# Kernel tuning notes

Hardware: AMD Instinct MI355X
Metric: run time of the kernel (lower is better)

Reference implementation:

```python
import jax, jax.numpy as jnp
import numpy as np

B, M, K = 32768, 8192, 16
EPS = 1e-5  # torch BatchNorm1d default


def _bn_relu(x, g, b):
    # training-mode batch norm (biased variance), matching torch BatchNorm1d forward
    m = x.mean(0)
    v = x.var(0)
    return jax.nn.relu(g * (x - m) * jax.lax.rsqrt(v + EPS) + b)


def _forward(pos, mc, mv, w1, b1, w2, b2, w3, b3, w4, b4, w5, b5, w6, b6,
             g1, be1, g2, be2, g3, be3, g4, be4, g5, be5, k):
    # squared pairwise distances [B, M]; same ordering as L2 norm used by torch.sort
    d2 = (pos * pos).sum(1, keepdims=True) + (mc * mc).sum(1)[None, :] - 2.0 * (pos @ mc.T)
    _, idx = jax.lax.top_k(-d2, k)                     # k nearest indices [B, k]
    nb = jnp.concatenate([mc[idx], mv[idx]], axis=-1)  # [B, k, 4] = (coord, value) per neighbor
    knn_feat = jnp.concatenate([pos, nb.reshape(pos.shape[0], k * 4)], axis=1)  # [B, 2+4k]
    x = _bn_relu(knn_feat @ w1 + b1, g1, be1)
    x = _bn_relu(x @ w2 + b2, g2, be2)
    x = _bn_relu(x @ w3 + b3, g3, be3)
    x = _bn_relu(x @ w4 + b4, g4, be4)
    x = _bn_relu(x @ w5 + b5, g5, be5)  # dropout = identity (eval mode)
    x = x @ w6 + b6
    return x, knn_feat


def setup_inputs() -> dict:
    key = jax.random.key(0)
    ks = jax.random.split(key, 32)
    d_in = 2 + K * 4
    dims = [(d_in, 128), (128, 256), (256, 512), (512, 128), (128, 64), (64, 2)]
    inp = {
        "pos": jax.random.normal(ks[0], (B, 2), jnp.float32),
        "measure_coords": jax.random.normal(ks[1], (M, 2), jnp.float32),
        "measure_vals": jax.random.normal(ks[2], (M, 2), jnp.float32),
    }
    for i, (fi, fo) in enumerate(dims, 1):
        inp[f"w{i}"] = jax.random.normal(ks[2 + 2 * i], (fi, fo), jnp.float32) / np.float32(np.sqrt(fi))
        inp[f"b{i}"] = jnp.zeros((fo,), jnp.float32)
    for i, n in enumerate([128, 256, 512, 128, 64], 1):
        inp[f"g{i}"] = jnp.ones((n,), jnp.float32)
        inp[f"be{i}"] = jnp.zeros((n,), jnp.float32)
    inp["k"] = K
    return inp


def reference(pos, measure_coords, measure_vals, w1, b1, w2, b2, w3, b3, w4, b4,
              w5, b5, w6, b6, g1, be1, g2, be2, g3, be3, g4, be4, g5, be5, k):
    return _forward(pos, measure_coords, measure_vals, w1, b1, w2, b2, w3, b3, w4,
                    b4, w5, b5, w6, b6, g1, be1, g2, be2, g3, be3, g4, be4, g5, be5, k)
```

## Files before the change

### kernel.cpp

```cpp
#include <hip/hip_runtime.h>

typedef unsigned short u16;
typedef unsigned int   u32;
typedef __attribute__((ext_vector_type(8))) short bf16x8;
typedef __attribute__((ext_vector_type(4))) float f32x4;

#define B_ROWS 32768
#define EPS_BN 1e-5f

__device__ __forceinline__ u16 f2bf(float f) {
  u32 u = __float_as_uint(f);
  u32 r = (u + 0x7FFFu + ((u >> 16) & 1u)) >> 16;
  return (u16)r;
}
__device__ __forceinline__ u32 pk2bf(float a, float b) {
  return (u32)f2bf(a) | ((u32)f2bf(b) << 16);
}
__device__ __forceinline__ float bf2f(u16 h) {
  return __uint_as_float(((u32)h) << 16);
}

__device__ __forceinline__ float dcalc(float px, float py, float sp, float mx, float my) {
#pragma clang fp contract(off)
  float sm   = mx * mx + my * my;
  float pm   = px * mx;
  float dot  = __builtin_fmaf(py, my, pm);
  float spsm = sp + sm;
  return __builtin_fmaf(dot, -2.0f, spsm);
}
__device__ __forceinline__ float dcalc2(float px, float py, float sp, float mx, float my,
                                        float sm) {
#pragma clang fp contract(off)
  float pm   = px * mx;
  float dot  = __builtin_fmaf(py, my, pm);
  float spsm = sp + sm;
  return __builtin_fmaf(dot, -2.0f, spsm);
}
__device__ __forceinline__ float smcalc(float mx, float my) {
#pragma clang fp contract(off)
  return mx * mx + my * my;
}
__device__ __forceinline__ float spcalc(float px, float py) {
#pragma clang fp contract(off)
  return px * px + py * py;
}
#define MED3 __builtin_amdgcn_fmed3f

__global__ __launch_bounds__(256, 8)
void knn_kernel(const float2* __restrict__ pos, const float2* __restrict__ mc,
                const float2* __restrict__ mv, float* __restrict__ knn_out,
                u16* __restrict__ X0)
{
  __shared__ float tv[16 * 65];
  __shared__ float tstS[16];
  __shared__ float qxS[16], qyS[16], qsS[16];
  __shared__ unsigned long long qmaskS[16];
  __shared__ int   qcnt[16];
  __shared__ int   ntaskS;

  const int t = threadIdx.x;
  const int g = t >> 6;
  const int s = t & 63;
  const int q0 = blockIdx.x * 16;

  float px[4], py[4], sp[4];
#pragma unroll
  for (int j = 0; j < 4; ++j) {
    float2 p = pos[q0 + g * 4 + j];
    px[j] = p.x; py[j] = p.y; sp[j] = spcalc(p.x, p.y);
  }
#pragma unroll
  for (int j = 0; j < 4; ++j) {
    if (s == j) { qxS[g * 4 + j] = px[j]; qyS[g * 4 + j] = py[j]; qsS[g * 4 + j] = sp[j]; }
  }

  const float4* mc4 = (const float4*)mc;

  float z0a[4], z0b[4];
#pragma unroll
  for (int j = 0; j < 4; ++j) { z0a[j] = __builtin_inff(); z0b[j] = __builtin_inff(); }

  float4 cur = mc4[s];
  for (int i = 0; i < 64; ++i) {
    float4 nxt = mc4[((i + 1) & 63) * 64 + s];
    float smA = smcalc(cur.x, cur.y);
    float smB = smcalc(cur.z, cur.w);
#pragma unroll
    for (int j = 0; j < 4; ++j) {
      float dA = dcalc2(px[j], py[j], sp[j], cur.x, cur.y, smA);
      z0a[j] = fminf(z0a[j], dA);
      float dB = dcalc2(px[j], py[j], sp[j], cur.z, cur.w, smB);
      z0b[j] = fminf(z0b[j], dB);
    }
    cur = nxt;
  }
  float z0[4];
#pragma unroll
  for (int j = 0; j < 4; ++j) {
    z0[j] = fminf(z0a[j], z0b[j]);
    tv[(g * 4 + j) * 65 + s] = z0[j];
  }
  __syncthreads();

  if (t < 16) {
    float ch[16];
#pragma unroll
    for (int j = 0; j < 16; ++j) ch[j] = __builtin_inff();
    for (int k = 0; k < 64; ++k) {
      float v = tv[t * 65 + k];
#pragma unroll
      for (int j = 15; j >= 1; --j) ch[j] = MED3(ch[j-1], v, ch[j]);
      ch[0] = fminf(ch[0], v);
    }
    tstS[t] = ch[15];
    qcnt[t] = 0;
    if (t == 0) ntaskS = 0;
  }
  __syncthreads();

  {
    float Tq[4];
#pragma unroll
    for (int j = 0; j < 4; ++j) Tq[j] = tstS[g * 4 + j];
    unsigned long long m;
#pragma unroll
    for (int j = 0; j < 4; ++j) {
      m = __ballot(z0[j] <= Tq[j]);
      if (s == j) qmaskS[g * 4 + j] = m;
    }
  }
  __syncthreads();

  u16* qcand = (u16*)tv;
  u16* taskS = ((u16*)tv) + 1024;
  if (t < 16) {
    unsigned long long m = qmaskS[t];
    int c = __popcll(m);
    int off = atomicAdd(&ntaskS, c);
    u16 qb = (u16)(t << 6);
    while (m) {
      int b = (int)__builtin_ctzll(m);
      m &= m - 1;
      taskS[off++] = qb | (u16)b;
    }
  }
  __syncthreads();

  const int ntask = ntaskS;
  for (int i0 = t; i0 < ntask; i0 += 256) {
    const int task = taskS[i0];
    const int qrow = task >> 6;
    const int sl   = task & 63;
    const float qx = qxS[qrow], qy = qyS[qrow];
    const float qs = qsS[qrow], qT = tstS[qrow];
#pragma unroll 4
    for (int i = 0; i < 64; ++i) {
      float4 c2 = mc4[i * 64 + sl];
      const int pidx = 2 * (i * 64 + sl);
      float smA = smcalc(c2.x, c2.y);
      float smB = smcalc(c2.z, c2.w);
      float dA = dcalc2(qx, qy, qs, c2.x, c2.y, smA);
      float dB = dcalc2(qx, qy, qs, c2.z, c2.w, smB);
      if (dA <= qT) {
        int o = atomicAdd(&qcnt[qrow], 1);
        if (o < 64) qcand[qrow * 64 + o] = (u16)pidx;
      }
      if (dB <= qT) {
        int o = atomicAdd(&qcnt[qrow], 1);
        if (o < 64) qcand[qrow * 64 + o] = (u16)(pidx + 1);
      }
    }
  }
  __syncthreads();

  if (t < 16) {
    const int q = q0 + t;
    float2 p = pos[q];
    const float sq = spcalc(p.x, p.y);
    int cnt = qcnt[t]; if (cnt > 64) cnt = 64;
    float fd[16]; int fi[16];
#pragma unroll
    for (int j = 0; j < 16; ++j) { fd[j] = __builtin_inff(); fi[j] = 0x7fffffff; }
    for (int j = 0; j < cnt; ++j) {
      int ci = qcand[t * 64 + j];
      float2 m = mc[ci];
      float d = dcalc(p.x, p.y, sq, m.x, m.y);
      bool cc = (d < fd[15]) || (d == fd[15] && ci < fi[15]);
      if (cc) {
#pragma unroll
        for (int k = 15; k >= 1; --k) {
          bool cm = (d < fd[k-1]) || (d == fd[k-1] && ci < fi[k-1]);
          if (cc) {
            if (cm) { fd[k] = fd[k-1]; fi[k] = fi[k-1]; }
            else    { fd[k] = d;       fi[k] = ci;      }
          }
          cc = cm;
        }
        if (cc) { fd[0] = d; fi[0] = ci; }
      }
    }
    float* orow = knn_out + (size_t)q * 66;
    u16*   xrow = X0 + (size_t)q * 96;
    float2 pp; pp.x = p.x; pp.y = p.y;
    *(float2*)(&orow[0]) = pp;
    *(u32*)(&xrow[0]) = pk2bf(p.x, p.y);
#pragma unroll
    for (int j = 0; j < 16; ++j) {
      int ci = fi[j];
      float2 m = mc[ci], v = mv[ci];
      *(float2*)(&orow[2 + 4*j]) = m;
      *(float2*)(&orow[4 + 4*j]) = v;
      *(u32*)(&xrow[2 + 4*j]) = pk2bf(m.x, m.y);
      *(u32*)(&xrow[4 + 4*j]) = pk2bf(v.x, v.y);
    }
#pragma unroll
    for (int c = 33; c < 48; ++c) ((u32*)xrow)[c] = 0;
  }
}

__global__ __launch_bounds__(256)
void prep_wt_all(const float* __restrict__ w1, const float* __restrict__ w2,
                 const float* __restrict__ w3, const float* __restrict__ w4,
                 const float* __restrict__ w5,
                 u16* __restrict__ wt1, u16* __restrict__ wt2, u16* __restrict__ wt3,
                 u16* __restrict__ wt4, u16* __restrict__ wt5)
{
  const int l = blockIdx.y;
  const float* w; u16* wt; int K, N, Kp;
  if (l == 0)      { w = w1; wt = wt1; K = 66;  N = 128; Kp = 96;  }
  else if (l == 1) { w = w2; wt = wt2; K = 128; N = 256; Kp = 128; }
  else if (l == 2) { w = w3; wt = wt3; K = 256; N = 512; Kp = 256; }
  else if (l == 3) { w = w4; wt = wt4; K = 512; N = 128; Kp = 512; }
  else             { w = w5; wt = wt5; K = 128; N = 64;  Kp = 128; }
  int i = blockIdx.x * 256 + threadIdx.x;
  if (i >= N * Kp) return;
  int n = i / Kp, kp = i - n * Kp;
  float v = (kp < K) ? w[(size_t)kp * N + n] : 0.0f;
  wt[i] = f2bf(v);
}

template<int KW, int BN, bool FUSE>
__global__ __launch_bounds__(256, 4)
void gemm_bn_kernel(const u16* __restrict__ X,
                    const u16* __restrict__ WT,
                    const float* __restrict__ bias,
                    const float* __restrict__ psum, const float* __restrict__ psq,
                    const float* __restrict__ gw,   const float* __restrict__ bw,
                    u16* __restrict__ Z, int N,
                    float* __restrict__ csum, float* __restrict__ csq)
{
  constexpr int BM = 128;
  constexpr int AST = 40;
  constexpr int NSTEP = KW / 32;
  __shared__ u16 Ash[2][BM * AST];
  __shared__ u16 Bsh[2][BN * AST];
  __shared__ float redS[4][BN];
  __shared__ float redQ[4][BN];
  __shared__ float scA[FUSE ? KW : 1];
  __shared__ float ttA[FUSE ? KW : 1];

  const int t = threadIdx.x;
  const int wave = t >> 6;
  const int lane = t & 63;
  const int lr = lane & 15;
  const int qd = lane >> 4;
  const int m0 = blockIdx.x * BM;
  const int n0 = blockIdx.y * BN;

  if (FUSE) {
    const float invB = 1.0f / 32768.0f;
    for (int c = t; c < KW; c += 256) {
      float mean = psum[c] * invB;
      float var  = __fmaf_rn(-mean, mean, psq[c] * invB);
      float sc   = gw[c] * rsqrtf(var + EPS_BN);
      scA[c] = sc;
      ttA[c] = __fmaf_rn(-mean, sc, bw[c]);
    }
    __syncthreads();
  }

  f32x4 acc[2][BN / 16];
#pragma unroll
  for (int a = 0; a < 2; ++a)
#pragma unroll
    for (int b = 0; b < BN / 16; ++b) {
      acc[a][b][0] = 0.f; acc[a][b][1] = 0.f; acc[a][b][2] = 0.f; acc[a][b][3] = 0.f;
    }

  const int sr = t >> 2;
  const int sk = (t & 3) * 8;

  const u16* Arow0 = &X[(size_t)(m0 + sr) * KW + sk];
  const u16* Arow1 = &X[(size_t)(m0 + sr + 64) * KW + sk];
  const u16* Brow  = &WT[(size_t)(n0 + sr) * KW + sk];

  auto fuseq = [&](uint4 gv, int kk) -> uint4 {
    u32 w[4] = {gv.x, gv.y, gv.z, gv.w};
    u32 o[4];
#pragma unroll
    for (int e = 0; e < 4; ++e) {
      float lo = bf2f((u16)(w[e] & 0xffffu));
      float hi = bf2f((u16)(w[e] >> 16));
      float yl = fmaxf(__fmaf_rn(lo, scA[kk + 2 * e],     ttA[kk + 2 * e]),     0.0f);
      float yh = fmaxf(__fmaf_rn(hi, scA[kk + 2 * e + 1], ttA[kk + 2 * e + 1]), 0.0f);
      o[e] = (u32)f2bf(yl) | ((u32)f2bf(yh) << 16);
    }
    uint4 r; r.x = o[0]; r.y = o[1]; r.z = o[2]; r.w = o[3];
    return r;
  };

  {
    uint4 a0 = *(const uint4*)(Arow0);
    uint4 a1 = *(const uint4*)(Arow1);
    uint4 b0 = *(const uint4*)(Brow);
    if (FUSE) { a0 = fuseq(a0, sk); a1 = fuseq(a1, sk); }
    *(uint4*)(&Ash[0][sr * AST + sk]) = a0;
    *(uint4*)(&Ash[0][(sr + 64) * AST + sk]) = a1;
    *(uint4*)(&Bsh[0][sr * AST + sk]) = b0;
  }
  uint4 a0n = {}, a1n = {}, b0n = {};
  if (NSTEP > 1) {
    a0n = *(const uint4*)(Arow0 + 32);
    a1n = *(const uint4*)(Arow1 + 32);
    b0n = *(const uint4*)(Brow + 32);
  }
  __syncthreads();

  for (int ts = 0; ts < NSTEP; ++ts) {
    const int cur = ts & 1;

    uint4 La0 = a0n, La1 = a1n, Lb0 = b0n;
    if (ts + 2 < NSTEP) {
      const int ko = (ts + 2) * 32;
      La0 = *(const uint4*)(Arow0 + ko);
      La1 = *(const uint4*)(Arow1 + ko);
      Lb0 = *(const uint4*)(Brow + ko);
    }

    bf16x8 af0 = *(const bf16x8*)(&Ash[cur][(wave * 32 + lr) * AST + qd * 8]);
    bf16x8 af1 = *(const bf16x8*)(&Ash[cur][(wave * 32 + 16 + lr) * AST + qd * 8]);
#pragma unroll
    for (int ct = 0; ct < BN / 16; ++ct) {
      bf16x8 bfr = *(const bf16x8*)(&Bsh[cur][(ct * 16 + lr) * AST + qd * 8]);
      acc[0][ct] = __builtin_amdgcn_mfma_f32_16x16x32_bf16(af0, bfr, acc[0][ct], 0, 0, 0);
      acc[1][ct] = __builtin_amdgcn_mfma_f32_16x16x32_bf16(af1, bfr, acc[1][ct], 0, 0, 0);
    }

    if (ts + 1 < NSTEP) {
      uint4 wa0 = a0n, wa1 = a1n, wb0 = b0n;
      if (FUSE) {
        const int kk = (ts + 1) * 32 + sk;
        wa0 = fuseq(wa0, kk);
        wa1 = fuseq(wa1, kk);
      }
      *(uint4*)(&Ash[cur ^ 1][sr * AST + sk]) = wa0;
      *(uint4*)(&Ash[cur ^ 1][(sr + 64) * AST + sk]) = wa1;
      *(uint4*)(&Bsh[cur ^ 1][sr * AST + sk]) = wb0;
      __syncthreads();
      a0n = La0; a1n = La1; b0n = Lb0;
    }
  }

#pragma unroll
  for (int ct = 0; ct < BN / 16; ++ct) {
    int cg = n0 + ct * 16 + lr;
    float bv = bias[cg];
    float s = 0.f, sqv = 0.f;
#pragma unroll
    for (int rt = 0; rt < 2; ++rt) {
#pragma unroll
      for (int r = 0; r < 4; ++r) {
        float z = acc[rt][ct][r] + bv;
        int row = m0 + wave * 32 + rt * 16 + qd * 4 + r;
        Z[(size_t)row * N + cg] = f2bf(z);
        s += z;
        sqv = __fmaf_rn(z, z, sqv);
      }
    }
    s   += __shfl_xor(s, 16);   s   += __shfl_xor(s, 32);
    sqv += __shfl_xor(sqv, 16); sqv += __shfl_xor(sqv, 32);
    if (qd == 0) { redS[wave][ct * 16 + lr] = s; redQ[wave][ct * 16 + lr] = sqv; }
  }
  __syncthreads();
  if (t < BN) {
    float s  = redS[0][t] + redS[1][t] + redS[2][t] + redS[3][t];
    float sv = redQ[0][t] + redQ[1][t] + redQ[2][t] + redQ[3][t];
    atomicAdd(&csum[n0 + t], s);
    atomicAdd(&csq[n0 + t], sv);
  }
}

__global__ __launch_bounds__(256)
void gemv6_kernel(const u16* __restrict__ Z5, const float* __restrict__ w6,
                  const float* __restrict__ b6,
                  const float* __restrict__ psum, const float* __restrict__ psq,
                  const float* __restrict__ gw,   const float* __restrict__ bw,
                  float* __restrict__ out)
{
  __shared__ float wsh[128];
  __shared__ float scs[64];
  __shared__ float tts[64];
  const int t = threadIdx.x;
  if (t < 128) wsh[t] = w6[t];
  if (t < 64) {
    const float invB = 1.0f / 32768.0f;
    float mean = psum[t] * invB;
    float var  = __fmaf_rn(-mean, mean, psq[t] * invB);
    float sc   = gw[t] * rsqrtf(var + EPS_BN);
    scs[t] = sc;
    tts[t] = __fmaf_rn(-mean, sc, bw[t]);
  }
  __syncthreads();
  const int q = blockIdx.x * 256 + t;
  const uint4* xv = (const uint4*)(Z5 + (size_t)q * 64);
  float a0 = 0.f, a1 = 0.f;
#pragma unroll
  for (int cc = 0; cc < 8; ++cc) {
    uint4 pk = xv[cc];
    u32 u[4] = {pk.x, pk.y, pk.z, pk.w};
#pragma unroll
    for (int uu = 0; uu < 4; ++uu) {
      int k = cc * 8 + uu * 2;
      float z0 = bf2f((u16)(u[uu] & 0xffffu));
      float z1 = bf2f((u16)(u[uu] >> 16));
      float x0 = fmaxf(__fmaf_rn(z0, scs[k],     tts[k]),     0.0f);
      float x1 = fmaxf(__fmaf_rn(z1, scs[k + 1], tts[k + 1]), 0.0f);
      x0 = bf2f(f2bf(x0));
      x1 = bf2f(f2bf(x1));
      a0 = __fmaf_rn(x0, wsh[2 * k + 0], a0);
      a1 = __fmaf_rn(x0, wsh[2 * k + 1], a1);
      a0 = __fmaf_rn(x1, wsh[2 * k + 2], a0);
      a1 = __fmaf_rn(x1, wsh[2 * k + 3], a1);
    }
  }
  float2 o; o.x = a0 + b6[0]; o.y = a1 + b6[1];
  ((float2*)out)[q] = o;
}

extern "C" void kernel_launch(void* const* d_in, const int* in_sizes, int n_in,
                              void* d_out, int out_size, void* d_ws, size_t ws_size,
                              hipStream_t stream)
{
  const float2* pos = (const float2*)d_in[0];
  const float2* mc  = (const float2*)d_in[1];
  const float2* mv  = (const float2*)d_in[2];
  const float* w1 = (const float*)d_in[3];  const float* b1 = (const float*)d_in[4];
  const float* w2 = (const float*)d_in[5];  const float* b2 = (const float*)d_in[6];
  const float* w3 = (const float*)d_in[7];  const float* b3 = (const float*)d_in[8];
  const float* w4 = (const float*)d_in[9];  const float* b4 = (const float*)d_in[10];
  const float* w5 = (const float*)d_in[11]; const float* b5 = (const float*)d_in[12];
  const float* w6 = (const float*)d_in[13]; const float* b6 = (const float*)d_in[14];
  const float* g1 = (const float*)d_in[15]; const float* be1 = (const float*)d_in[16];
  const float* g2 = (const float*)d_in[17]; const float* be2 = (const float*)d_in[18];
  const float* g3 = (const float*)d_in[19]; const float* be3 = (const float*)d_in[20];
  const float* g4 = (const float*)d_in[21]; const float* be4 = (const float*)d_in[22];
  const float* g5 = (const float*)d_in[23]; const float* be5 = (const float*)d_in[24];

  char* ws = (char*)d_ws;
  u16* X0   = (u16*)(ws + 0);
  u16* ZA   = (u16*)(ws + 6291456);
  u16* ZB   = (u16*)(ws + 39845888);
  u16* WT1  = (u16*)(ws + 73400320);
  u16* WT2  = (u16*)(ws + 73424896);
  u16* WT3  = (u16*)(ws + 73490432);
  u16* WT4  = (u16*)(ws + 73752576);
  u16* WT5  = (u16*)(ws + 73883648);
  float* stats = (float*)(ws + 73900032);
  float* s1 = stats;        float* s2 = stats + 128;  float* s3 = stats + 384;
  float* s4 = stats + 896;  float* s5 = stats + 1024;
  float* sqb = stats + 1088;
  float* q1 = sqb;          float* q2 = sqb + 128;    float* q3 = sqb + 384;
  float* q4 = sqb + 896;    float* q5 = sqb + 1024;

  float* outX = (float*)d_out;
  float* outK = outX + 2 * B_ROWS;

  hipMemsetAsync(stats, 0, 2176 * sizeof(float), stream);
  prep_wt_all<<<dim3(512, 5), 256, 0, stream>>>(w1, w2, w3, w4, w5, WT1, WT2, WT3, WT4, WT5);
  knn_kernel<<<dim3(2048), 256, 0, stream>>>(pos, mc, mv, outK, X0);

  gemm_bn_kernel<96,  64, false><<<dim3(256, 2), 256, 0, stream>>>(
      X0, WT1, b1, nullptr, nullptr, nullptr, nullptr, ZA, 128, s1, q1);
  gemm_bn_kernel<128, 64, true><<<dim3(256, 4), 256, 0, stream>>>(
      ZA, WT2, b2, s1, q1, g1, be1, ZB, 256, s2, q2);
  gemm_bn_kernel<256, 64, true><<<dim3(256, 8), 256, 0, stream>>>(
      ZB, WT3, b3, s2, q2, g2, be2, ZA, 512, s3, q3);
  gemm_bn_kernel<512, 64, true><<<dim3(256, 2), 256, 0, stream>>>(
      ZA, WT4, b4, s3, q3, g3, be3, ZB, 128, s4, q4);
  gemm_bn_kernel<128, 64, true><<<dim3(256, 1), 256, 0, stream>>>(
      ZB, WT5, b5, s4, q4, g4, be4, ZA, 64, s5, q5);
  gemv6_kernel<<<dim3(128), 256, 0, stream>>>(ZA, w6, b6, s5, q5, g5, be5, outX);

  (void)in_sizes; (void)n_in; (void)out_size; (void)ws_size;
}
```

Before: 300.3 us.

## Fold weight prep and stats zeroing into knn kernel; vectorize distance loop with packed f32x2

Removes the separate memset and prep_wt_all launches by having the knn kernel zero the BN stats and convert all weights to transposed bf16 with grid-stride loops before its main work. The knn distance loop is rewritten with 2-wide float vectors so the compiler can emit packed FP32 math for the two candidates per load. The BN template parameter of the GEMM is also hardcoded to 64, which is cleanup. This saves two launches and may double distance throughput, at the cost of extra prologue work in every knn block.

Measured after the change: 308.6 us. +2.8%, slower.

```diff
diff --git a/kernel.cpp b/kernel.cpp
--- a/kernel.cpp
+++ b/kernel.cpp
@@ -4,6 +4,7 @@
 typedef unsigned int   u32;
 typedef __attribute__((ext_vector_type(8))) short bf16x8;
 typedef __attribute__((ext_vector_type(4))) float f32x4;
+typedef __attribute__((ext_vector_type(2))) float f32x2;
 
 #define B_ROWS 32768
 #define EPS_BN 1e-5f
@@ -19,6 +20,7 @@
 __device__ __forceinline__ float bf2f(u16 h) {
   return __uint_as_float(((u32)h) << 16);
 }
+__device__ __forceinline__ f32x2 splat2(float v) { f32x2 r; r.x = v; r.y = v; return r; }
 
 __device__ __forceinline__ float dcalc(float px, float py, float sp, float mx, float my) {
 #pragma clang fp contract(off)
@@ -44,12 +46,32 @@
 #pragma clang fp contract(off)
   return px * px + py * py;
 }
+__device__ __forceinline__ f32x2 smcalc2(f32x2 mx, f32x2 my) {
+#pragma clang fp contract(off)
+  f32x2 a = mx * mx;
+  f32x2 b = my * my;
+  return a + b;
+}
+__device__ __forceinline__ f32x2 dcalc2v(float px, float py, float sp,
+                                         f32x2 mx, f32x2 my, f32x2 sm) {
+#pragma clang fp contract(off)
+  f32x2 pm   = splat2(px) * mx;
+  f32x2 dot  = __builtin_elementwise_fma(splat2(py), my, pm);
+  f32x2 spsm = splat2(sp) + sm;
+  return __builtin_elementwise_fma(dot, splat2(-2.0f), spsm);
+}
 #define MED3 __builtin_amdgcn_fmed3f
 
 __global__ __launch_bounds__(256, 8)
 void knn_kernel(const float2* __restrict__ pos, const float2* __restrict__ mc,
                 const float2* __restrict__ mv, float* __restrict__ knn_out,
-                u16* __restrict__ X0)
+                u16* __restrict__ X0,
+                const float* __restrict__ w1, const float* __restrict__ w2,
+                const float* __restrict__ w3, const float* __restrict__ w4,
+                const float* __restrict__ w5,
+                u16* __restrict__ WT1, u16* __restrict__ WT2, u16* __restrict__ WT3,
+                u16* __restrict__ WT4, u16* __restrict__ WT5,
+                float* __restrict__ stats)
 {
   __shared__ float tv[16 * 65];
   __shared__ float tstS[16];
@@ -63,6 +85,32 @@
   const int s = t & 63;
   const int q0 = blockIdx.x * 16;
 
+  {
+    const int gid = blockIdx.x * 256 + t;
+    const int gs  = gridDim.x * 256;
+    for (int i = gid; i < 2176; i += gs) stats[i] = 0.f;
+    for (int i = gid; i < 128 * 96; i += gs) {
+      int n = i / 96, kp = i - n * 96;
+      WT1[i] = f2bf((kp < 66) ? w1[(size_t)kp * 128 + n] : 0.0f);
+    }
+    for (int i = gid; i < 256 * 128; i += gs) {
+      int n = i >> 7, kp = i & 127;
+      WT2[i] = f2bf(w2[(size_t)kp * 256 + n]);
+    }
+    for (int i = gid; i < 512 * 256; i += gs) {
+      int n = i >> 8, kp = i & 255;
+      WT3[i] = f2bf(w3[(size_t)kp * 512 + n]);
+    }
+    for (int i = gid; i < 128 * 512; i += gs) {
+      int n = i >> 9, kp = i & 511;
+      WT4[i] = f2bf(w4[(size_t)kp * 128 + n]);
+    }
+    for (int i = gid; i < 64 * 128; i += gs) {
+      int n = i >> 7, kp = i & 127;
+      WT5[i] = f2bf(w5[(size_t)kp * 64 + n]);
+    }
+  }
+
   float px[4], py[4], sp[4];
 #pragma unroll
   for (int j = 0; j < 4; ++j) {
@@ -76,28 +124,27 @@
 
   const float4* mc4 = (const float4*)mc;
 
-  float z0a[4], z0b[4];
-#pragma unroll
-  for (int j = 0; j < 4; ++j) { z0a[j] = __builtin_inff(); z0b[j] = __builtin_inff(); }
+  f32x2 z2[4];
+#pragma unroll
+  for (int j = 0; j < 4; ++j) { z2[j].x = __builtin_inff(); z2[j].y = __builtin_inff(); }
 
   float4 cur = mc4[s];
   for (int i = 0; i < 64; ++i) {
     float4 nxt = mc4[((i + 1) & 63) * 64 + s];
-    float smA = smcalc(cur.x, cur.y);
-    float smB = smcalc(cur.z, cur.w);
+    f32x2 mx; mx.x = cur.x; mx.y = cur.z;
+    f32x2 my; my.x = cur.y; my.y = cur.w;
+    f32x2 sm2 = smcalc2(mx, my);
 #pragma unroll
     for (int j = 0; j < 4; ++j) {
-      float dA = dcalc2(px[j], py[j], sp[j], cur.x, cur.y, smA);
-      z0a[j] = fminf(z0a[j], dA);
-      float dB = dcalc2(px[j], py[j], sp[j], cur.z, cur.w, smB);
-      z0b[j] = fminf(z0b[j], dB);
+      f32x2 d2 = dcalc2v(px[j], py[j], sp[j], mx, my, sm2);
+      z2[j] = __builtin_elementwise_min(z2[j], d2);
     }
     cur = nxt;
   }
   float z0[4];
 #pragma unroll
   for (int j = 0; j < 4; ++j) {
-    z0[j] = fminf(z0a[j], z0b[j]);
+    z0[j] = fminf(z2[j].x, z2[j].y);
     tv[(g * 4 + j) * 65 + s] = z0[j];
   }
   __syncthreads();
@@ -218,28 +265,7 @@
   }
 }
 
-__global__ __launch_bounds__(256)
-void prep_wt_all(const float* __restrict__ w1, const float* __restrict__ w2,
-                 const float* __restrict__ w3, const float* __restrict__ w4,
-                 const float* __restrict__ w5,
-                 u16* __restrict__ wt1, u16* __restrict__ wt2, u16* __restrict__ wt3,
-                 u16* __restrict__ wt4, u16* __restrict__ wt5)
-{
-  const int l = blockIdx.y;
-  const float* w; u16* wt; int K, N, Kp;
-  if (l == 0)      { w = w1; wt = wt1; K = 66;  N = 128; Kp = 96;  }
-  else if (l == 1) { w = w2; wt = wt2; K = 128; N = 256; Kp = 128; }
-  else if (l == 2) { w = w3; wt = wt3; K = 256; N = 512; Kp = 256; }
-  else if (l == 3) { w = w4; wt = wt4; K = 512; N = 128; Kp = 512; }
-  else             { w = w5; wt = wt5; K = 128; N = 64;  Kp = 128; }
-  int i = blockIdx.x * 256 + threadIdx.x;
-  if (i >= N * Kp) return;
-  int n = i / Kp, kp = i - n * Kp;
-  float v = (kp < K) ? w[(size_t)kp * N + n] : 0.0f;
-  wt[i] = f2bf(v);
-}
-
-template<int KW, int BN, bool FUSE>
+template<int KW, bool FUSE>
 __global__ __launch_bounds__(256, 4)
 void gemm_bn_kernel(const u16* __restrict__ X,
                     const u16* __restrict__ WT,
@@ -253,9 +279,9 @@
   constexpr int AST = 40;
   constexpr int NSTEP = KW / 32;
   __shared__ u16 Ash[2][BM * AST];
-  __shared__ u16 Bsh[2][BN * AST];
-  __shared__ float redS[4][BN];
-  __shared__ float redQ[4][BN];
+  __shared__ u16 Bsh[2][64 * AST];
+  __shared__ float redS[4][64];
+  __shared__ float redQ[4][64];
   __shared__ float scA[FUSE ? KW : 1];
   __shared__ float ttA[FUSE ? KW : 1];
 
@@ -265,7 +291,7 @@
   const int lr = lane & 15;
   const int qd = lane >> 4;
   const int m0 = blockIdx.x * BM;
-  const int n0 = blockIdx.y * BN;
+  const int n0 = blockIdx.y * 64;
 
   if (FUSE) {
     const float invB = 1.0f / 32768.0f;
@@ -279,11 +305,11 @@
     __syncthreads();
   }
 
-  f32x4 acc[2][BN / 16];
+  f32x4 acc[2][4];
 #pragma unroll
   for (int a = 0; a < 2; ++a)
 #pragma unroll
-    for (int b = 0; b < BN / 16; ++b) {
+    for (int b = 0; b < 4; ++b) {
       acc[a][b][0] = 0.f; acc[a][b][1] = 0.f; acc[a][b][2] = 0.f; acc[a][b][3] = 0.f;
     }
 
@@ -340,7 +366,7 @@
     bf16x8 af0 = *(const bf16x8*)(&Ash[cur][(wave * 32 + lr) * AST + qd * 8]);
     bf16x8 af1 = *(const bf16x8*)(&Ash[cur][(wave * 32 + 16 + lr) * AST + qd * 8]);
 #pragma unroll
-    for (int ct = 0; ct < BN / 16; ++ct) {
+    for (int ct = 0; ct < 4; ++ct) {
       bf16x8 bfr = *(const bf16x8*)(&Bsh[cur][(ct * 16 + lr) * AST + qd * 8]);
       acc[0][ct] = __builtin_amdgcn_mfma_f32_16x16x32_bf16(af0, bfr, acc[0][ct], 0, 0, 0);
       acc[1][ct] = __builtin_amdgcn_mfma_f32_16x16x32_bf16(af1, bfr, acc[1][ct], 0, 0, 0);
@@ -362,7 +388,7 @@
   }
 
 #pragma unroll
-  for (int ct = 0; ct < BN / 16; ++ct) {
+  for (int ct = 0; ct < 4; ++ct) {
     int cg = n0 + ct * 16 + lr;
     float bv = bias[cg];
     float s = 0.f, sqv = 0.f;
@@ -382,7 +408,7 @@
     if (qd == 0) { redS[wave][ct * 16 + lr] = s; redQ[wave][ct * 16 + lr] = sqv; }
   }
   __syncthreads();
-  if (t < BN) {
+  if (t < 64) {
     float s  = redS[0][t] + redS[1][t] + redS[2][t] + redS[3][t];
     float sv = redQ[0][t] + redQ[1][t] + redQ[2][t] + redQ[3][t];
     atomicAdd(&csum[n0 + t], s);
@@ -475,19 +501,19 @@
   float* outX = (float*)d_out;
   float* outK = outX + 2 * B_ROWS;
 
-  hipMemsetAsync(stats, 0, 2176 * sizeof(float), stream);
-  prep_wt_all<<<dim3(512, 5), 256, 0, stream>>>(w1, w2, w3, w4, w5, WT1, WT2, WT3, WT4, WT5);
-  knn_kernel<<<dim3(2048), 256, 0, stream>>>(pos, mc, mv, outK, X0);
-
-  gemm_bn_kernel<96,  64, false><<<dim3(256, 2), 256, 0, stream>>>(
+  knn_kernel<<<dim3(2048), 256, 0, stream>>>(pos, mc, mv, outK, X0,
+                                             w1, w2, w3, w4, w5,
+                                             WT1, WT2, WT3, WT4, WT5, stats);
+
+  gemm_bn_kernel<96,  false><<<dim3(256, 2), 256, 0, stream>>>(
       X0, WT1, b1, nullptr, nullptr, nullptr, nullptr, ZA, 128, s1, q1);
-  gemm_bn_kernel<128, 64, true><<<dim3(256, 4), 256, 0, stream>>>(
+  gemm_bn_kernel<128, true><<<dim3(256, 4), 256, 0, stream>>>(
       ZA, WT2, b2, s1, q1, g1, be1, ZB, 256, s2, q2);
-  gemm_bn_kernel<256, 64, true><<<dim3(256, 8), 256, 0, stream>>>(
+  gemm_bn_kernel<256, true><<<dim3(256, 8), 256, 0, stream>>>(
       ZB, WT3, b3, s2, q2, g2, be2, ZA, 512, s3, q3);
-  gemm_bn_kernel<512, 64, true><<<dim3(256, 2), 256, 0, stream>>>(
+  gemm_bn_kernel<512, true><<<dim3(256, 2), 256, 0, stream>>>(
       ZA, WT4, b4, s3, q3, g3, be3, ZB, 128, s4, q4);
-  gemm_bn_kernel<128, 64, true><<<dim3(256, 1), 256, 0, stream>>>(
+  gemm_bn_kernel<128, true><<<dim3(256, 1), 256, 0, stream>>>(
       ZB, WT5, b5, s4, q4, g4, be4, ZA, 64, s5, q5);
   gemv6_kernel<<<dim3(128), 256, 0, stream>>>(ZA, w6, b6, s5, q5, g5, be5, outX);
 
```
